# Kernel optimization log

Measured on AMD Instinct MI355X. Metric: run time of the kernel, lower is better.

The kernel has to match this reference:

```python
import jax, jax.numpy as jnp
import numpy as np

B, T, D, N = 4, 2048, 1024, 16

def setup_inputs() -> dict:
    key = jax.random.key(0)
    ks = jax.random.split(key, 6)
    scale = 0.02
    return {
        'x': jax.random.normal(ks[0], (B, T, D), dtype=jnp.float32),
        'Wd': jax.random.normal(ks[1], (D, D), dtype=jnp.float32) * (1.0 / np.sqrt(D)),
        'bd': jnp.zeros((D,), dtype=jnp.float32),
        'a_log': jax.random.normal(ks[2], (D, N), dtype=jnp.float32) * scale,
        'b_param': jax.random.normal(ks[3], (D, N), dtype=jnp.float32) * scale,
        'Wo': jax.random.normal(ks[4], (D, D), dtype=jnp.float32) * (1.0 / np.sqrt(D)),
        'bo': jnp.zeros((D,), dtype=jnp.float32),
    }

def reference(x, Wd, bd, a_log, b_param, Wo, bo):
    # delta: [B,T,D]
    delta = jax.nn.softplus(jnp.einsum('btd,ed->bte', x, Wd) + bd)
    a_pos = jax.nn.softplus(a_log) + 1e-4  # [D,N]

    def step(state, inputs):
        x_t, delta_t = inputs  # [B,D], [B,D]
        dt = delta_t[..., None]                      # [B,D,1]
        a_bar = jnp.exp(-dt * a_pos)                 # [B,D,N]
        state = a_bar * state + (dt * b_param) * x_t[..., None]
        return state, state.sum(axis=-1)             # y_t: [B,D]

    init = jnp.zeros((B, D, N), dtype=x.dtype)
    xs = (jnp.swapaxes(x, 0, 1), jnp.swapaxes(delta, 0, 1))  # [T,B,D]
    _, y = jax.lax.scan(step, init, xs)              # y: [T,B,D]
    y = jnp.swapaxes(y, 0, 1)                        # [B,T,D]
    return jnp.einsum('btd,ed->bte', y, Wo) + bo
```

## Files before the change

### kernel.cpp

```cpp
#include <hip/hip_runtime.h>
#include <hip/hip_bf16.h>

#define B_ 4
#define T_ 2048
#define D_ 1024
#define N_ 16
#define TCH 32
#define NCH 64

#define GM 8192
#define GK 1024
#define GN 1024

typedef __attribute__((ext_vector_type(4))) float f32x4;
typedef __attribute__((ext_vector_type(8))) short short8;
typedef unsigned int u32;
typedef unsigned short u16;

#if defined(__has_builtin)
#if __has_builtin(__builtin_amdgcn_exp2f)
#define EXP2(x) __builtin_amdgcn_exp2f(x)
#else
#define EXP2(x) exp2f(x)
#endif
#else
#define EXP2(x) exp2f(x)
#endif

__device__ __forceinline__ float softplus_f(float v) {
    return v > 20.f ? v : log1pf(__expf(v));
}

__device__ __forceinline__ u16 f2bf(float f) {
    u32 u = __float_as_uint(f);
    u32 r = (u + 0x7fffu + ((u >> 16) & 1u)) >> 16;
    return (u16)r;
}

__global__ __launch_bounds__(256) void cvt_f32_bf16(const float* __restrict__ in,
                                                    u16* __restrict__ out, int n4) {
    int i = blockIdx.x * 256 + threadIdx.x;
    if (i >= n4) return;
    float4 v = ((const float4*)in)[i];
    ushort4 o;
    o.x = f2bf(v.x); o.y = f2bf(v.y); o.z = f2bf(v.z); o.w = f2bf(v.w);
    ((ushort4*)out)[i] = o;
}

__device__ __forceinline__ void gload_lds16(const void* g, void* l) {
    __builtin_amdgcn_global_load_lds((const __attribute__((address_space(1))) u32*)g,
                                     (__attribute__((address_space(3))) u32*)l, 16, 0, 0);
}

template <int ACT>
__global__ __launch_bounds__(512, 6) void gemm_bt(const u16* __restrict__ A,
                                                  const u16* __restrict__ Bw,
                                                  const float* __restrict__ bias,
                                                  float* __restrict__ C) {
    __shared__ __align__(16) u16 sA[2][64 * 64];
    __shared__ __align__(16) u16 sB[2][128 * 64];
    const int tid = threadIdx.x;
    const int wid = tid >> 6;
    const int lane = tid & 63;

    const int wg = blockIdx.x;
    const int xcd = wg & 7;
    const int jj = wg >> 3;
    const int bx = xcd * 16 + (jj & 15);
    const int by = jj >> 4;
    const int m0 = bx * 64;
    const int n0 = by * 128;
    const int wm = wid >> 2;
    const int wn = wid & 3;

    const int lrow = lane >> 3;
    const int slot = lane & 7;
    const int ksw = (slot ^ lrow) << 3;

    const u16* aP  = A  + (size_t)(m0 + wid * 8 + lrow) * GK + ksw;
    const u16* bP0 = Bw + (size_t)(n0 + wid * 8 + lrow) * GK + ksw;
    const u16* bP1 = Bw + (size_t)(n0 + (wid + 8) * 8 + lrow) * GK + ksw;
    const int ldsA  = wid * 1024;
    const int ldsB1 = (wid + 8) * 1024;

    f32x4 acc[2][2] = {};
    const int fr = lane & 15;
    const int g = lane >> 4;
    const int xorv = (fr & 7) << 4;

    gload_lds16(aP,  (char*)sA[0] + ldsA);
    gload_lds16(bP0, (char*)sB[0] + ldsA);
    gload_lds16(bP1, (char*)sB[0] + ldsB1);

    #pragma unroll
    for (int t = 0; t < GK / 64; ++t) {
        __syncthreads();
        if (t + 1 < GK / 64) {
            const int nb = (t + 1) & 1;
            gload_lds16(aP  + (t + 1) * 64, (char*)sA[nb] + ldsA);
            gload_lds16(bP0 + (t + 1) * 64, (char*)sB[nb] + ldsA);
            gload_lds16(bP1 + (t + 1) * 64, (char*)sB[nb] + ldsB1);
        }
        const char* bA = (const char*)sA[t & 1];
        const char* bB = (const char*)sB[t & 1];
        #pragma unroll
        for (int kk = 0; kk < 2; ++kk) {
            const int ksb = (kk * 64 + g * 16) ^ xorv;
            short8 af[2], bf[2];
            #pragma unroll
            for (int f = 0; f < 2; ++f)
                af[f] = *(const short8*)(bA + (wm * 32 + f * 16 + fr) * 128 + ksb);
            #pragma unroll
            for (int f = 0; f < 2; ++f)
                bf[f] = *(const short8*)(bB + (wn * 32 + f * 16 + fr) * 128 + ksb);
            __builtin_amdgcn_s_setprio(1);
            #pragma unroll
            for (int i = 0; i < 2; ++i)
                #pragma unroll
                for (int j2 = 0; j2 < 2; ++j2)
                    acc[i][j2] = __builtin_amdgcn_mfma_f32_16x16x32_bf16(af[i], bf[j2],
                                                                         acc[i][j2], 0, 0, 0);
            __builtin_amdgcn_s_setprio(0);
        }
    }

    const int cl = lane & 15;
    const int rg = (lane >> 4) * 4;
    #pragma unroll
    for (int j2 = 0; j2 < 2; ++j2) {
        const int col = n0 + wn * 32 + j2 * 16 + cl;
        const float bv = bias[col];
        #pragma unroll
        for (int i = 0; i < 2; ++i) {
            #pragma unroll
            for (int r = 0; r < 4; ++r) {
                const int rowg = m0 + wm * 32 + i * 16 + rg + r;
                float v = acc[i][j2][r] + bv;
                if (ACT) v = softplus_f(v);
                C[(size_t)rowg * GN + col] = v;
            }
        }
    }
}

__global__ __launch_bounds__(256) void scan_p1(const float* __restrict__ delta,
                                               const float* __restrict__ x,
                                               const float* __restrict__ a_log,
                                               float* __restrict__ S,
                                               float* __restrict__ dtsum) {
    const int gid = blockIdx.x * 256 + threadIdx.x;
    const int lane = gid & 63;
    const int w = gid >> 6;
    const int dw = w & 31;
    const int cb = w >> 5;
    const int d = dw * 32 + (lane & 31);
    const int half = lane >> 5;
    const int b = cb & (B_ - 1);
    const int c = cb >> 2;

    float an2[8];
    {
        const float4* a4 = (const float4*)&a_log[d * N_ + half * 8];
        float4 a0 = a4[0], a1 = a4[1];
        an2[0] = (softplus_f(a0.x) + 1e-4f) * 1.44269504f;
        an2[1] = (softplus_f(a0.y) + 1e-4f) * 1.44269504f;
        an2[2] = (softplus_f(a0.z) + 1e-4f) * 1.44269504f;
        an2[3] = (softplus_f(a0.w) + 1e-4f) * 1.44269504f;
        an2[4] = (softplus_f(a1.x) + 1e-4f) * 1.44269504f;
        an2[5] = (softplus_f(a1.y) + 1e-4f) * 1.44269504f;
        an2[6] = (softplus_f(a1.z) + 1e-4f) * 1.44269504f;
        an2[7] = (softplus_f(a1.w) + 1e-4f) * 1.44269504f;
    }

    float s[8];
    #pragma unroll
    for (int n = 0; n < 8; ++n) s[n] = 0.f;
    float dts = 0.f;

    const size_t base = ((size_t)b * T_ + (size_t)c * TCH) * D_ + d;
    for (int i = 0; i < TCH; ++i) {
        const float dt = delta[base + (size_t)i * D_];
        const float xv = x[base + (size_t)i * D_];
        const float dtx = dt * xv;
        dts += dt;
        #pragma unroll
        for (int n = 0; n < 8; ++n) {
            const float ab = EXP2(-dt * an2[n]);
            s[n] = fmaf(ab, s[n], dtx);
        }
    }

    float4* So = (float4*)&S[((size_t)cb * D_ + d) * N_ + half * 8];
    So[0] = make_float4(s[0], s[1], s[2], s[3]);
    So[1] = make_float4(s[4], s[5], s[6], s[7]);
    if (half == 0) dtsum[(size_t)cb * D_ + d] = dts;
}

__global__ __launch_bounds__(256) void scan_p2(const float* __restrict__ S,
                                               const float* __restrict__ dtsum,
                                               const float* __restrict__ a_log,
                                               float* __restrict__ carry_out) {
    const int gid = blockIdx.x * 256 + threadIdx.x;
    const int n = gid & 15;
    const int d = (gid >> 4) & (D_ - 1);
    const int b = gid >> 14;
    const float an2 = (softplus_f(a_log[d * N_ + n]) + 1e-4f) * 1.44269504f;
    float carry = 0.f;
    for (int c = 0; c < NCH; ++c) {
        const size_t cb = (size_t)c * B_ + b;
        const size_t idx = (cb * D_ + d) * N_ + n;
        carry_out[idx] = carry;
        const float dts = dtsum[cb * D_ + d];
        const float P = EXP2(-dts * an2);
        carry = fmaf(P, carry, S[idx]);
    }
}

__global__ __launch_bounds__(256) void scan_p3(const float* __restrict__ delta,
                                               const float* __restrict__ x,
                                               const float* __restrict__ a_log,
                                               const float* __restrict__ b_param,
                                               const float* __restrict__ carry_in,
                                               u16* __restrict__ y) {
    const int gid = blockIdx.x * 256 + threadIdx.x;
    const int lane = gid & 63;
    const int w = gid >> 6;
    const int dw = w & 31;
    const int cb = w >> 5;
    const int d = dw * 32 + (lane & 31);
    const int half = lane >> 5;
    const int b = cb & (B_ - 1);
    const int c = cb >> 2;

    float an2[8], bp[8];
    {
        const float4* a4 = (const float4*)&a_log[d * N_ + half * 8];
        const float4* b4 = (const float4*)&b_param[d * N_ + half * 8];
        float4 a0 = a4[0], a1 = a4[1];
        float4 v0 = b4[0], v1 = b4[1];
        an2[0] = (softplus_f(a0.x) + 1e-4f) * 1.44269504f;
        an2[1] = (softplus_f(a0.y) + 1e-4f) * 1.44269504f;
        an2[2] = (softplus_f(a0.z) + 1e-4f) * 1.44269504f;
        an2[3] = (softplus_f(a0.w) + 1e-4f) * 1.44269504f;
        an2[4] = (softplus_f(a1.x) + 1e-4f) * 1.44269504f;
        an2[5] = (softplus_f(a1.y) + 1e-4f) * 1.44269504f;
        an2[6] = (softplus_f(a1.z) + 1e-4f) * 1.44269504f;
        an2[7] = (softplus_f(a1.w) + 1e-4f) * 1.44269504f;
        bp[0] = v0.x; bp[1] = v0.y; bp[2] = v0.z; bp[3] = v0.w;
        bp[4] = v1.x; bp[5] = v1.y; bp[6] = v1.z; bp[7] = v1.w;
    }

    float s[8];
    {
        const float4* ci = (const float4*)&carry_in[((size_t)cb * D_ + d) * N_ + half * 8];
        float4 c0 = ci[0], c1 = ci[1];
        s[0] = c0.x; s[1] = c0.y; s[2] = c0.z; s[3] = c0.w;
        s[4] = c1.x; s[5] = c1.y; s[6] = c1.z; s[7] = c1.w;
    }

    const size_t base = ((size_t)b * T_ + (size_t)c * TCH) * D_ + d;
    for (int i = 0; i < TCH; ++i) {
        const float dt = delta[base + (size_t)i * D_];
        const float xv = x[base + (size_t)i * D_];
        const float dtx = dt * xv;
        float acc = 0.f;
        #pragma unroll
        for (int n = 0; n < 8; ++n) {
            const float ab = EXP2(-dt * an2[n]);
            s[n] = fmaf(ab, s[n], dtx);
            acc = fmaf(bp[n], s[n], acc);
        }
        const float tot = acc + __shfl_xor(acc, 32);
        if (half == 0) y[base + (size_t)i * D_] = f2bf(tot);
    }
}

extern "C" void kernel_launch(void* const* d_in, const int* in_sizes, int n_in,
                              void* d_out, int out_size, void* d_ws, size_t ws_size,
                              hipStream_t stream) {
    const float* x      = (const float*)d_in[0];
    const float* Wd     = (const float*)d_in[1];
    const float* bd     = (const float*)d_in[2];
    const float* a_log  = (const float*)d_in[3];
    const float* b_par  = (const float*)d_in[4];
    const float* Wo     = (const float*)d_in[5];
    const float* bo     = (const float*)d_in[6];
    float* out = (float*)d_out;

    char* ws = (char*)d_ws;
    u16*   xbf     = (u16*)(ws);
    float* carry   = (float*)(ws);
    float* S       = (float*)(ws + 16777216);
    u16*   ybf     = (u16*)(ws + 16777216);
    float* delta   = (float*)(ws + 33554432);
    u16*   wdbf    = (u16*)(ws + 67108864);
    u16*   wobf    = (u16*)(ws + 69206016);
    float* dtsum   = (float*)(ws + 71303168);
    (void)in_sizes; (void)n_in; (void)out_size; (void)ws_size;

    const int M = B_ * T_;

    cvt_f32_bf16<<<(M * D_ / 4 + 255) / 256, 256, 0, stream>>>(x, xbf, M * D_ / 4);
    cvt_f32_bf16<<<(D_ * D_ / 4 + 255) / 256, 256, 0, stream>>>(Wd, wdbf, D_ * D_ / 4);
    cvt_f32_bf16<<<(D_ * D_ / 4 + 255) / 256, 256, 0, stream>>>(Wo, wobf, D_ * D_ / 4);

    gemm_bt<1><<<(GM / 64) * (GN / 128), 512, 0, stream>>>(xbf, wdbf, bd, delta);

    scan_p1<<<NCH * B_ * D_ * 2 / 256, 256, 0, stream>>>(delta, x, a_log, S, dtsum);
    scan_p2<<<B_ * D_ * N_ / 256, 256, 0, stream>>>(S, dtsum, a_log, carry);
    scan_p3<<<NCH * B_ * D_ * 2 / 256, 256, 0, stream>>>(delta, x, a_log, b_par, carry, ybf);

    gemm_bt<0><<<(GM / 64) * (GN / 128), 512, 0, stream>>>(ybf, wobf, bo, out);
}
```

Before: 176.1 us.

## Replace LDS double buffer with register-staged prefetch in GEMM

```diff
diff --git a/kernel.cpp b/kernel.cpp
--- a/kernel.cpp
+++ b/kernel.cpp
@@ -47,18 +47,13 @@
     ((ushort4*)out)[i] = o;
 }
 
-__device__ __forceinline__ void gload_lds16(const void* g, void* l) {
-    __builtin_amdgcn_global_load_lds((const __attribute__((address_space(1))) u32*)g,
-                                     (__attribute__((address_space(3))) u32*)l, 16, 0, 0);
-}
-
 template <int ACT>
-__global__ __launch_bounds__(512, 6) void gemm_bt(const u16* __restrict__ A,
+__global__ __launch_bounds__(512, 8) void gemm_bt(const u16* __restrict__ A,
                                                   const u16* __restrict__ Bw,
                                                   const float* __restrict__ bias,
                                                   float* __restrict__ C) {
-    __shared__ __align__(16) u16 sA[2][64 * 64];
-    __shared__ __align__(16) u16 sB[2][128 * 64];
+    __shared__ __align__(16) u16 sA[64 * 64];
+    __shared__ __align__(16) u16 sB[128 * 64];
     const int tid = threadIdx.x;
     const int wid = tid >> 6;
     const int lane = tid & 63;
@@ -80,39 +75,48 @@
     const u16* aP  = A  + (size_t)(m0 + wid * 8 + lrow) * GK + ksw;
     const u16* bP0 = Bw + (size_t)(n0 + wid * 8 + lrow) * GK + ksw;
     const u16* bP1 = Bw + (size_t)(n0 + (wid + 8) * 8 + lrow) * GK + ksw;
-    const int ldsA  = wid * 1024;
-    const int ldsB1 = (wid + 8) * 1024;
-
-    f32x4 acc[2][2] = {};
+
+    const int wOff = wid * 1024 + lrow * 128 + slot * 16;
+    char* const wA  = (char*)sA + wOff;
+    char* const wB  = (char*)sB + wOff;
+
     const int fr = lane & 15;
     const int g = lane >> 4;
     const int xorv = (fr & 7) << 4;
-
-    gload_lds16(aP,  (char*)sA[0] + ldsA);
-    gload_lds16(bP0, (char*)sB[0] + ldsA);
-    gload_lds16(bP1, (char*)sB[0] + ldsB1);
+    const char* const rA0 = (const char*)sA + (wm * 32 + fr) * 128 + ((g * 16) ^ xorv);
+    const char* const rA1 = (const char*)sA + (wm * 32 + fr) * 128 + ((64 + g * 16) ^ xorv);
+    const char* const rB0 = (const char*)sB + (wn * 32 + fr) * 128 + ((g * 16) ^ xorv);
+    const char* const rB1 = (const char*)sB + (wn * 32 + fr) * 128 + ((64 + g * 16) ^ xorv);
+
+    short8 ra, rb0, rb1;
+    f32x4 acc[2][2] = {};
+
+    ra  = *(const short8*)(aP);
+    rb0 = *(const short8*)(bP0);
+    rb1 = *(const short8*)(bP1);
+    *(short8*)(wA)        = ra;
+    *(short8*)(wB)        = rb0;
+    *(short8*)(wB + 8192) = rb1;
+    ra  = *(const short8*)(aP + 64);
+    rb0 = *(const short8*)(bP0 + 64);
+    rb1 = *(const short8*)(bP1 + 64);
+    asm volatile("s_waitcnt lgkmcnt(0)" ::: "memory");
+    __builtin_amdgcn_s_barrier();
+    asm volatile("" ::: "memory");
 
     #pragma unroll
     for (int t = 0; t < GK / 64; ++t) {
-        __syncthreads();
-        if (t + 1 < GK / 64) {
-            const int nb = (t + 1) & 1;
-            gload_lds16(aP  + (t + 1) * 64, (char*)sA[nb] + ldsA);
-            gload_lds16(bP0 + (t + 1) * 64, (char*)sB[nb] + ldsA);
-            gload_lds16(bP1 + (t + 1) * 64, (char*)sB[nb] + ldsB1);
-        }
-        const char* bA = (const char*)sA[t & 1];
-        const char* bB = (const char*)sB[t & 1];
         #pragma unroll
         for (int kk = 0; kk < 2; ++kk) {
-            const int ksb = (kk * 64 + g * 16) ^ xorv;
+            const char* bA = kk ? rA1 : rA0;
+            const char* bB = kk ? rB1 : rB0;
             short8 af[2], bf[2];
             #pragma unroll
             for (int f = 0; f < 2; ++f)
-                af[f] = *(const short8*)(bA + (wm * 32 + f * 16 + fr) * 128 + ksb);
+                af[f] = *(const short8*)(bA + f * 2048);
             #pragma unroll
             for (int f = 0; f < 2; ++f)
-                bf[f] = *(const short8*)(bB + (wn * 32 + f * 16 + fr) * 128 + ksb);
+                bf[f] = *(const short8*)(bB + f * 2048);
             __builtin_amdgcn_s_setprio(1);
             #pragma unroll
             for (int i = 0; i < 2; ++i)
@@ -121,6 +125,22 @@
                     acc[i][j2] = __builtin_amdgcn_mfma_f32_16x16x32_bf16(af[i], bf[j2],
                                                                          acc[i][j2], 0, 0, 0);
             __builtin_amdgcn_s_setprio(0);
+        }
+        if (t + 1 < GK / 64) {
+            asm volatile("s_waitcnt lgkmcnt(0)" ::: "memory");
+            __builtin_amdgcn_s_barrier();
+            asm volatile("" ::: "memory");
+            *(short8*)(wA)        = ra;
+            *(short8*)(wB)        = rb0;
+            *(short8*)(wB + 8192) = rb1;
+            asm volatile("s_waitcnt lgkmcnt(0)" ::: "memory");
+            __builtin_amdgcn_s_barrier();
+            asm volatile("" ::: "memory");
+            if (t + 2 < GK / 64) {
+                ra  = *(const short8*)(aP  + (t + 2) * 64);
+                rb0 = *(const short8*)(bP0 + (t + 2) * 64);
+                rb1 = *(const short8*)(bP1 + (t + 2) * 64);
+            }
         }
     }
 
```

Measured after the change: 171.1 us. 2.8% less time.
